# Performance work log

Measured on AMD Instinct MI355X. Metric: run time of the kernel, lower is better.

The kernel has to match this reference:

```python
import jax, jax.numpy as jnp
import numpy as np

N_NODES = 100000
N_EDGES = 3200000
IN_FEATS = 128
H_FEATS = 256
REG_NUM = 1


def _linear_params(key, fan_in, fan_out):
    kw, kb = jax.random.split(key)
    bound = 1.0 / np.sqrt(fan_in)
    W = jax.random.uniform(kw, (fan_out, fan_in), minval=-bound, maxval=bound, dtype=jnp.float32)
    b = jax.random.uniform(kb, (fan_out,), minval=-bound, maxval=bound, dtype=jnp.float32)
    return W, b


def setup_inputs() -> dict:
    key = jax.random.key(0)
    ks = jax.random.split(key, 12)
    node_feat = jax.random.normal(ks[0], (N_NODES, IN_FEATS), dtype=jnp.float32)
    edge_feat = jax.random.normal(ks[1], (N_EDGES, 1), dtype=jnp.float32)
    edge_dst = jax.random.randint(ks[2], (N_EDGES,), 0, N_NODES, dtype=jnp.int64)
    # SAGE layer weights: conv1 maps in_feats+1 -> h_feats; mids map h_feats+1 -> h_feats
    W1, b1 = _linear_params(ks[3], IN_FEATS + 1, H_FEATS)
    Wm1, bm1 = _linear_params(ks[4], H_FEATS + 1, H_FEATS)
    Wm2, bm2 = _linear_params(ks[5], H_FEATS + 1, H_FEATS)
    Wm3, bm3 = _linear_params(ks[6], H_FEATS + 1, H_FEATS)
    Wm4, bm4 = _linear_params(ks[7], H_FEATS + 1, H_FEATS)
    Wr1, br1 = _linear_params(ks[8], H_FEATS + 1, H_FEATS)
    Wr2, br2 = _linear_params(ks[9], H_FEATS, H_FEATS)
    Wr3, br3 = _linear_params(ks[10], H_FEATS, REG_NUM)
    return {
        "node_feat": node_feat, "edge_feat": edge_feat, "edge_dst": edge_dst,
        "W1": W1, "b1": b1,
        "Wm1": Wm1, "bm1": bm1, "Wm2": Wm2, "bm2": bm2,
        "Wm3": Wm3, "bm3": bm3, "Wm4": Wm4, "bm4": bm4,
        "Wr1": Wr1, "br1": br1, "Wr2": Wr2, "br2": br2, "Wr3": Wr3, "br3": br3,
    }


def _sage_layer(hn, he_aggr, W, b):
    # concat [N, d] with [N, 1] then linear
    h_total = jnp.concatenate([hn, he_aggr], axis=1)
    return h_total @ W.T + b


def reference(node_feat, edge_feat, edge_dst,
              W1, b1, Wm1, bm1, Wm2, bm2, Wm3, bm3, Wm4, bm4,
              Wr1, br1, Wr2, br2, Wr3, br3):
    # copy_e + sum: scatter-add edge features onto destination nodes -> [N, 1]
    he_aggr = jax.ops.segment_sum(edge_feat, edge_dst, num_segments=N_NODES)
    h = jax.nn.relu(_sage_layer(node_feat, he_aggr, W1, b1))  # dropout = identity (eval)
    h = jax.nn.relu(_sage_layer(h, he_aggr, Wm1, bm1))
    h = jax.nn.relu(_sage_layer(h, he_aggr, Wm2, bm2))
    h = jax.nn.relu(_sage_layer(h, he_aggr, Wm3, bm3))
    h = jax.nn.relu(_sage_layer(h, he_aggr, Wm4, bm4))
    h = jax.nn.relu(_sage_layer(h, he_aggr, Wr1, br1))
    h = jax.nn.relu(h @ Wr2.T + br2)
    return h @ Wr3.T + br3
```

## Files before the change

kernel.cpp:

```cpp
#include <hip/hip_runtime.h>
#include <hip/hip_bf16.h>

typedef _Float16 half8  __attribute__((ext_vector_type(8)));
typedef _Float16 half4v __attribute__((ext_vector_type(4)));
typedef float    f32x4  __attribute__((ext_vector_type(4)));

#define N_NODES 100000
#define N_EDGES 3200000
#define SH_STRIDE 100096
#define NBUCK 782
#define CAP   5120
#define CHUNK 4096
#define NBIN  782
#define NPK   32

__global__ __launch_bounds__(512) void binpack(
    const float* __restrict__ ef, const int* __restrict__ dst,
    const float* __restrict__ W1,  const float* __restrict__ Wm1,
    const float* __restrict__ Wm2, const float* __restrict__ Wm3,
    const float* __restrict__ Wm4, const float* __restrict__ Wr1,
    const float* __restrict__ Wr2,
    const float* __restrict__ b1,  const float* __restrict__ bm1,
    const float* __restrict__ bm2, const float* __restrict__ bm3,
    const float* __restrict__ bm4, const float* __restrict__ br1,
    const float* __restrict__ br2, const float* __restrict__ wr3,
    const float* __restrict__ br3,
    int* __restrict__ cursor, unsigned* __restrict__ pairs,
    _Float16* __restrict__ Wp, float* __restrict__ park, int do_bin) {

    if (do_bin && blockIdx.x < NBIN) {
        __shared__ int      hist[NBUCK];
        __shared__ int      base[NBUCK];
        __shared__ int      lbase[NBUCK];
        __shared__ int      wsum[8];
        __shared__ unsigned lrec[CHUNK];
        __shared__ int      lslot[CHUNK];
        const int start = blockIdx.x * CHUNK;
        const int tid   = threadIdx.x;
        const int wave  = tid >> 6;
        const int lane  = tid & 63;
        for (int b = tid; b < NBUCK; b += 512) hist[b] = 0;
        __syncthreads();

        int4   dreg[2];
        float4 freg[2];
        int    rnk[2][4];
        #pragma unroll
        for (int it = 0; it < 2; ++it) {
            const int i = start + (it * 512 + tid) * 4;
            if (i < N_EDGES) {
                dreg[it] = *(const int4*)&dst[i];
                freg[it] = *(const float4*)&ef[i];
                rnk[it][0] = atomicAdd(&hist[dreg[it].x >> 7], 1);
                rnk[it][1] = atomicAdd(&hist[dreg[it].y >> 7], 1);
                rnk[it][2] = atomicAdd(&hist[dreg[it].z >> 7], 1);
                rnk[it][3] = atomicAdd(&hist[dreg[it].w >> 7], 1);
            }
        }
        __syncthreads();

        for (int b = tid; b < NBUCK; b += 512) {
            const int c = hist[b];
            base[b] = b * CAP + ((c > 0) ? atomicAdd(&cursor[b], c) : 0);
        }
        const int b0 = 2 * tid, b1 = 2 * tid + 1;
        const int h0 = (b0 < NBUCK) ? hist[b0] : 0;
        const int h1 = (b1 < NBUCK) ? hist[b1] : 0;
        const int psum = h0 + h1;
        int pfx = psum;
        #pragma unroll
        for (int ofs = 1; ofs < 64; ofs <<= 1) {
            const int v = __shfl_up(pfx, ofs);
            if (lane >= ofs) pfx += v;
        }
        if (lane == 63) wsum[wave] = pfx;
        __syncthreads();
        int woff = 0;
        #pragma unroll
        for (int w = 0; w < 8; ++w) woff += (w < wave) ? wsum[w] : 0;
        const int excl = woff + pfx - psum;
        if (b0 < NBUCK) lbase[b0] = excl;
        if (b1 < NBUCK) lbase[b1] = excl + h0;
        __syncthreads();

        #pragma unroll
        for (int it = 0; it < 2; ++it) {
            const int i = start + (it * 512 + tid) * 4;
            if (i < N_EDGES) {
                const int4   d = dreg[it];
                const float4 f = freg[it];
                {   const int bk = d.x >> 7; const int r = rnk[it][0];
                    const int s = lbase[bk] + r; const int g = base[bk] + r;
                    lrec[s]  = (__float_as_uint(f.x) & 0xFFFFFF00u) | (unsigned)(d.x & 127);
                    lslot[s] = (g < (bk + 1) * CAP) ? g : -1; }
                {   const int bk = d.y >> 7; const int r = rnk[it][1];
                    const int s = lbase[bk] + r; const int g = base[bk] + r;
                    lrec[s]  = (__float_as_uint(f.y) & 0xFFFFFF00u) | (unsigned)(d.y & 127);
                    lslot[s] = (g < (bk + 1) * CAP) ? g : -1; }
                {   const int bk = d.z >> 7; const int r = rnk[it][2];
                    const int s = lbase[bk] + r; const int g = base[bk] + r;
                    lrec[s]  = (__float_as_uint(f.z) & 0xFFFFFF00u) | (unsigned)(d.z & 127);
                    lslot[s] = (g < (bk + 1) * CAP) ? g : -1; }
                {   const int bk = d.w >> 7; const int r = rnk[it][3];
                    const int s = lbase[bk] + r; const int g = base[bk] + r;
                    lrec[s]  = (__float_as_uint(f.w) & 0xFFFFFF00u) | (unsigned)(d.w & 127);
                    lslot[s] = (g < (bk + 1) * CAP) ? g : -1; }
            }
        }
        __syncthreads();
        const int total = min(CHUNK, N_EDGES - start);
        for (int s = tid; s < total; s += 512) {
            const int g = lslot[s];
            if (g >= 0) pairs[g] = lrec[s];
        }
    } else {
        const float* srcs[7] = {W1, Wm1, Wm2, Wm3, Wm4, Wr1, Wr2};
        const float* bias[7] = {b1, bm1, bm2, bm3, bm4, br1, br2};
        const int pb  = do_bin ? ((int)blockIdx.x - NBIN) : (int)blockIdx.x;
        const int gid = pb * 512 + threadIdx.x;
        const int gsz = NPK * 512;
        for (int i = gid; i < 425984; i += gsz) {
            int job, w, s, j, lane, e, stride;
            if (i < 32768) {
                job = 0; stride = 129;
                w = i >> 13;
                const int rem = i & 8191;
                s = rem >> 11;
                j = (rem >> 9) & 3;
                lane = (rem >> 3) & 63;
                e = rem & 7;
            } else {
                const int t = i - 32768;
                job = 1 + (t >> 16);
                const int local = t & 65535;
                stride = (job == 6) ? 256 : 257;
                w = local >> 14;
                const int rem = local & 16383;
                s = rem >> 11;
                j = (rem >> 9) & 3;
                lane = (rem >> 3) & 63;
                e = rem & 7;
            }
            const int row = w * 64 + j * 16 + (lane & 15);
            const int col = s * 32 + ((lane >> 4) << 3) + e;
            Wp[i] = (_Float16)srcs[job][row * stride + col];
        }
        for (int i = gid; i < 1536; i += gsz) {
            const int job = i >> 8, row = i & 255;
            const int stride = (job == 0) ? 129 : 257;
            const int kin    = (job == 0) ? 128 : 256;
            park[job * 512 + row] = srcs[job][row * stride + kin];
        }
        for (int i = gid; i < 256; i += gsz) park[6 * 512 + i] = 0.f;
        for (int i = gid; i < 1792; i += gsz)
            park[(i >> 8) * 512 + 256 + (i & 255)] = bias[i >> 8][i & 255];
        for (int i = gid; i < 256; i += gsz) park[3584 + i] = wr3[i];
        if (gid == 0) park[3840] = br3[0];
    }
}

__global__ void scatter4(const float4* __restrict__ ef4,
                         const int4* __restrict__ dst4,
                         float* __restrict__ e) {
    const int n4 = N_EDGES / 4;
    for (int i = blockIdx.x * blockDim.x + threadIdx.x; i < n4;
         i += gridDim.x * blockDim.x) {
        const float4 f = ef4[i];
        const int4   d = dst4[i];
        atomicAdd(&e[d.x], f.x);
        atomicAdd(&e[SH_STRIDE + d.y], f.y);
        atomicAdd(&e[2 * SH_STRIDE + d.z], f.z);
        atomicAdd(&e[3 * SH_STRIDE + d.w], f.w);
    }
}

template<int K>
__device__ __forceinline__ void layer_mm(const _Float16* __restrict__ Wl,
                                         _Float16 (* __restrict__ Hs)[264],
                                         const float* __restrict__ es,
                                         const float* __restrict__ parkl,
                                         int wave, int lane, int m_, int quad) {
    f32x4 acc[4][8];
    #pragma unroll
    for (int jt = 0; jt < 4; ++jt)
        #pragma unroll
        for (int mt = 0; mt < 8; ++mt)
            acc[jt][mt] = (f32x4){0.f, 0.f, 0.f, 0.f};

    const int jb0 = wave * 64 + quad * 4;
    float4 w4[4], bb[4];
    #pragma unroll
    for (int jt = 0; jt < 4; ++jt) {
        w4[jt] = *(const float4*)&parkl[jt * 16 + jb0];
        bb[jt] = *(const float4*)&parkl[256 + jt * 16 + jb0];
    }

    const _Float16* __restrict__ wp = Wl + (size_t)wave * (64 * K) + lane * 8;

    half8 a[4];
    #pragma unroll
    for (int jt = 0; jt < 4; ++jt)
        a[jt] = *(const half8*)(wp + jt * 512);

    half8 b[8];
    #pragma unroll
    for (int mt = 0; mt < 8; ++mt)
        b[mt] = *(const half8*)&Hs[mt * 16 + m_][quad * 8];

    #pragma unroll
    for (int kk = 0; kk < K; kk += 32) {
        const int s = kk >> 5;
        half8 a2[4];
        if (kk + 32 < K) {
            #pragma unroll
            for (int jt = 0; jt < 4; ++jt)
                a2[jt] = *(const half8*)(wp + ((s + 1) * 4 + jt) * 512);
        }
        #pragma unroll
        for (int mt = 0; mt < 8; ++mt) {
            #pragma unroll
            for (int jt = 0; jt < 4; ++jt)
                acc[jt][mt] = __builtin_amdgcn_mfma_f32_16x16x32_f16(
                    a[jt], b[mt], acc[jt][mt], 0, 0, 0);
            if (kk + 32 < K)
                b[mt] = *(const half8*)&Hs[mt * 16 + m_][kk + 32 + quad * 8];
        }
        if (kk + 32 < K) {
            #pragma unroll
            for (int jt = 0; jt < 4; ++jt) a[jt] = a2[jt];
        }
    }
    __syncthreads();

    #pragma unroll
    for (int jt = 0; jt < 4; ++jt) {
        const int jbase = jb0 + jt * 16;
        #pragma unroll
        for (int mt = 0; mt < 8; ++mt) {
            const int node = mt * 16 + m_;
            const float ev = es[node];
            half4v h;
            h[0] = (_Float16)fmaxf(acc[jt][mt][0] + ev * w4[jt].x + bb[jt].x, 0.f);
            h[1] = (_Float16)fmaxf(acc[jt][mt][1] + ev * w4[jt].y + bb[jt].y, 0.f);
            h[2] = (_Float16)fmaxf(acc[jt][mt][2] + ev * w4[jt].z + bb[jt].z, 0.f);
            h[3] = (_Float16)fmaxf(acc[jt][mt][3] + ev * w4[jt].w + bb[jt].w, 0.f);
            *(half4v*)&Hs[node][jbase] = h;
        }
    }
    __syncthreads();
}

__global__ __launch_bounds__(256, 2) void sage_fused(
    const float* __restrict__ node_feat,
    const int* __restrict__ cursor, const unsigned* __restrict__ pairs,
    const float* __restrict__ esh, int nsh,
    const _Float16* __restrict__ Wpack, const float* __restrict__ park,
    float* __restrict__ out) {

    __shared__ _Float16 Hs[128][264];
    __shared__ float esp[528];
    __shared__ float es[128];
    __shared__ float wf[256];
    __shared__ float red[2][128];

    const int tid  = threadIdx.x;
    const int wave = tid >> 6;
    const int lane = tid & 63;
    const int m_   = lane & 15;
    const int quad = lane >> 4;
    const int node0 = blockIdx.x * 128;

    for (int i = tid; i < 528; i += 256) esp[i] = 0.f;

    int cnt = 0;
    if (nsh == 0) cnt = min(cursor[blockIdx.x], CAP);
    __syncthreads();

    for (int idx = tid; idx < 128 * 16; idx += 256) {
        const int row = idx >> 4, g = idx & 15;
        int node = node0 + row; if (node >= N_NODES) node = N_NODES - 1;
        const float4* src = (const float4*)(node_feat + (size_t)node * 128 + g * 8);
        const float4 v0 = src[0], v1 = src[1];
        half8 h;
        h[0] = (_Float16)v0.x; h[1] = (_Float16)v0.y;
        h[2] = (_Float16)v0.z; h[3] = (_Float16)v0.w;
        h[4] = (_Float16)v1.x; h[5] = (_Float16)v1.y;
        h[6] = (_Float16)v1.z; h[7] = (_Float16)v1.w;
        *(half8*)&Hs[row][g * 8] = h;
    }
    if (nsh != 0 && tid < 128) {
        int node = node0 + tid; if (node >= N_NODES) node = N_NODES - 1;
        float s = 0.f;
        for (int sh = 0; sh < nsh; ++sh) s += esh[(size_t)sh * SH_STRIDE + node];
        esp[tid] = s;
    }
    __syncthreads();

    {
        f32x4 acc[4][8];
        #pragma unroll
        for (int jt = 0; jt < 4; ++jt)
            #pragma unroll
            for (int mt = 0; mt < 8; ++mt)
                acc[jt][mt] = (f32x4){0.f, 0.f, 0.f, 0.f};

        const int jb0 = wave * 64 + quad * 4;
        float4 w4[4], bb4[4];
        #pragma unroll
        for (int jt = 0; jt < 4; ++jt) {
            w4[jt]  = *(const float4*)&park[jt * 16 + jb0];
            bb4[jt] = *(const float4*)&park[256 + jt * 16 + jb0];
        }

        const _Float16* __restrict__ wp =
            Wpack + (size_t)wave * (64 * 128) + lane * 8;
        half8 a[4];
        #pragma unroll
        for (int jt = 0; jt < 4; ++jt)
            a[jt] = *(const half8*)(wp + jt * 512);
        half8 b[8];
        #pragma unroll
        for (int mt = 0; mt < 8; ++mt)
            b[mt] = *(const half8*)&Hs[mt * 16 + m_][quad * 8];

        const unsigned* __restrict__ pp = pairs + (size_t)blockIdx.x * CAP;
        const int sh = (tid & 3) * 132;

        #pragma unroll
        for (int kk = 0; kk < 128; kk += 32) {
            const int s = kk >> 5;
            half8 a2[4];
            if (kk + 32 < 128) {
                #pragma unroll
                for (int jt = 0; jt < 4; ++jt)
                    a2[jt] = *(const half8*)(wp + ((s + 1) * 4 + jt) * 512);
            }
            if (nsh == 0) {
                for (int i = tid + (s << 8); i < cnt; i += 1024) {
                    const unsigned p = pp[i];
                    atomicAdd(&esp[sh + (p & 127u)],
                              __uint_as_float(p & 0xFFFFFF00u));
                }
            }
            #pragma unroll
            for (int mt = 0; mt < 8; ++mt) {
                #pragma unroll
                for (int jt = 0; jt < 4; ++jt)
                    acc[jt][mt] = __builtin_amdgcn_mfma_f32_16x16x32_f16(
                        a[jt], b[mt], acc[jt][mt], 0, 0, 0);
                if (kk + 32 < 128)
                    b[mt] = *(const half8*)&Hs[mt * 16 + m_][kk + 32 + quad * 8];
            }
            if (kk + 32 < 128) {
                #pragma unroll
                for (int jt = 0; jt < 4; ++jt) a[jt] = a2[jt];
            }
        }
        __syncthreads();
        if (tid < 128)
            es[tid] = esp[tid] + esp[132 + tid] + esp[264 + tid] + esp[396 + tid];
        __syncthreads();

        #pragma unroll
        for (int jt = 0; jt < 4; ++jt) {
            const int jbase = jb0 + jt * 16;
            #pragma unroll
            for (int mt = 0; mt < 8; ++mt) {
                const int node = mt * 16 + m_;
                const float ev = es[node];
                half4v h;
                h[0] = (_Float16)fmaxf(acc[jt][mt][0] + ev * w4[jt].x + bb4[jt].x, 0.f);
                h[1] = (_Float16)fmaxf(acc[jt][mt][1] + ev * w4[jt].y + bb4[jt].y, 0.f);
                h[2] = (_Float16)fmaxf(acc[jt][mt][2] + ev * w4[jt].z + bb4[jt].z, 0.f);
                h[3] = (_Float16)fmaxf(acc[jt][mt][3] + ev * w4[jt].w + bb4[jt].w, 0.f);
                *(half4v*)&Hs[node][jbase] = h;
            }
        }
        __syncthreads();
    }

    for (int l = 1; l < 7; ++l)
        layer_mm<256>(Wpack + 32768 + (l - 1) * 65536, Hs, es, park + l * 512,
                      wave, lane, m_, quad);

    wf[tid] = park[3584 + tid];
    __syncthreads();
    {
        const int row = tid & 127, seg = tid >> 7;
        const _Float16* hp = &Hs[row][seg * 128];
        const float* wpt = &wf[seg * 128];
        float s = 0.f;
        #pragma unroll
        for (int k = 0; k < 16; ++k) {
            const half8 h = *(const half8*)(hp + k * 8);
            const float* w8 = wpt + k * 8;
            s += (float)h[0] * w8[0] + (float)h[1] * w8[1]
               + (float)h[2] * w8[2] + (float)h[3] * w8[3]
               + (float)h[4] * w8[4] + (float)h[5] * w8[5]
               + (float)h[6] * w8[6] + (float)h[7] * w8[7];
        }
        red[seg][row] = s;
    }
    __syncthreads();
    if (tid < 128) {
        const int node = node0 + tid;
        if (node < N_NODES)
            out[node] = red[0][tid] + red[1][tid] + park[3840];
    }
}

extern "C" void kernel_launch(void* const* d_in, const int* in_sizes, int n_in,
                              void* d_out, int out_size, void* d_ws,
                              size_t ws_size, hipStream_t stream) {
    const float* node_feat = (const float*)d_in[0];
    const float* edge_feat = (const float*)d_in[1];
    const int*   edge_dst  = (const int*)d_in[2];
    const float* W1  = (const float*)d_in[3];  const float* b1  = (const float*)d_in[4];
    const float* Wm1 = (const float*)d_in[5];  const float* bm1 = (const float*)d_in[6];
    const float* Wm2 = (const float*)d_in[7];  const float* bm2 = (const float*)d_in[8];
    const float* Wm3 = (const float*)d_in[9];  const float* bm3 = (const float*)d_in[10];
    const float* Wm4 = (const float*)d_in[11]; const float* bm4 = (const float*)d_in[12];
    const float* Wr1 = (const float*)d_in[13]; const float* br1 = (const float*)d_in[14];
    const float* Wr2 = (const float*)d_in[15]; const float* br2 = (const float*)d_in[16];
    const float* Wr3 = (const float*)d_in[17]; const float* br3 = (const float*)d_in[18];
    float* out = (float*)d_out;

    char* ws = (char*)d_ws;
    int*      cursor = (int*)ws;
    _Float16* Wp     = (_Float16*)(ws + 4096);
    float*    park   = (float*)(ws + 856064);
    unsigned* pairs  = (unsigned*)(ws + 872448);
    float*    esh    = (float*)(ws + 872448);

    const size_t need_bins = 872448 + (size_t)NBUCK * CAP * 4;
    const bool use_bins = (ws_size >= need_bins);

    const int nblk = (N_NODES + 127) / 128;

    if (use_bins) {
        hipMemsetAsync(cursor, 0, NBUCK * sizeof(int), stream);
        binpack<<<NBIN + NPK, 512, 0, stream>>>(
            edge_feat, edge_dst, W1, Wm1, Wm2, Wm3, Wm4, Wr1, Wr2,
            b1, bm1, bm2, bm3, bm4, br1, br2, Wr3, br3,
            cursor, pairs, Wp, park, 1);
        sage_fused<<<nblk, 256, 0, stream>>>(node_feat, cursor, pairs,
                                             nullptr, 0, Wp, park, out);
    } else {
        binpack<<<NPK, 512, 0, stream>>>(
            edge_feat, edge_dst, W1, Wm1, Wm2, Wm3, Wm4, Wr1, Wr2,
            b1, bm1, bm2, bm3, bm4, br1, br2, Wr3, br3,
            cursor, pairs, Wp, park, 0);
        hipMemsetAsync(esh, 0, (size_t)4 * SH_STRIDE * 4, stream);
        scatter4<<<3125, 256, 0, stream>>>((const float4*)edge_feat,
                                           (const int4*)edge_dst, esh);
        sage_fused<<<nblk, 256, 0, stream>>>(node_feat, nullptr, nullptr,
                                             esh, 4, Wp, park, out);
    }
}
```

Baseline: 277.4 us.

## Retile fused SAGE GEMMs as 2x2 wave grid over nodes and output features

Each wave previously computed 64 output features for all 128 nodes, reading the full H tile from LDS. Now the four waves form a 2x2 grid, so each wave handles 64 nodes by 128 features. This halves per-wave LDS reads of the activations and doubles the per-wave weight fragments fetched from global/L2. The weight stream is now prefetched inside the MFMA loop in place of the LDS stream, with bias and edge-weight loads moved into the epilogue loop.

```diff
diff --git a/kernel.cpp b/kernel.cpp
--- a/kernel.cpp
+++ b/kernel.cpp
@@ -180,70 +180,70 @@
                                          const float* __restrict__ es,
                                          const float* __restrict__ parkl,
                                          int wave, int lane, int m_, int quad) {
-    f32x4 acc[4][8];
+    const int wr = wave >> 1, wc = wave & 1;
+    const int row0 = wr * 64;
+
+    f32x4 acc[8][4];
     #pragma unroll
-    for (int jt = 0; jt < 4; ++jt)
-        #pragma unroll
-        for (int mt = 0; mt < 8; ++mt)
+    for (int jt = 0; jt < 8; ++jt)
+        #pragma unroll
+        for (int mt = 0; mt < 4; ++mt)
             acc[jt][mt] = (f32x4){0.f, 0.f, 0.f, 0.f};
 
-    const int jb0 = wave * 64 + quad * 4;
-    float4 w4[4], bb[4];
+    const _Float16* __restrict__ wp = Wl + lane * 8;
+
+    half8 a[8];
     #pragma unroll
-    for (int jt = 0; jt < 4; ++jt) {
-        w4[jt] = *(const float4*)&parkl[jt * 16 + jb0];
-        bb[jt] = *(const float4*)&parkl[256 + jt * 16 + jb0];
-    }
-
-    const _Float16* __restrict__ wp = Wl + (size_t)wave * (64 * K) + lane * 8;
-
-    half8 a[4];
+    for (int jt = 0; jt < 8; ++jt)
+        a[jt] = *(const half8*)(wp + (size_t)(wc * 2 + (jt >> 2)) * (64 * K)
+                                + (jt & 3) * 512);
+
+    half8 b[4];
     #pragma unroll
-    for (int jt = 0; jt < 4; ++jt)
-        a[jt] = *(const half8*)(wp + jt * 512);
-
-    half8 b[8];
-    #pragma unroll
-    for (int mt = 0; mt < 8; ++mt)
-        b[mt] = *(const half8*)&Hs[mt * 16 + m_][quad * 8];
+    for (int mt = 0; mt < 4; ++mt)
+        b[mt] = *(const half8*)&Hs[row0 + mt * 16 + m_][quad * 8];
 
     #pragma unroll
     for (int kk = 0; kk < K; kk += 32) {
         const int s = kk >> 5;
-        half8 a2[4];
+        half8 b2[4];
         if (kk + 32 < K) {
             #pragma unroll
-            for (int jt = 0; jt < 4; ++jt)
-                a2[jt] = *(const half8*)(wp + ((s + 1) * 4 + jt) * 512);
-        }
-        #pragma unroll
-        for (int mt = 0; mt < 8; ++mt) {
-            #pragma unroll
-            for (int jt = 0; jt < 4; ++jt)
+            for (int mt = 0; mt < 4; ++mt)
+                b2[mt] = *(const half8*)&Hs[row0 + mt * 16 + m_][kk + 32 + quad * 8];
+        }
+        #pragma unroll
+        for (int jt = 0; jt < 8; ++jt) {
+            #pragma unroll
+            for (int mt = 0; mt < 4; ++mt)
                 acc[jt][mt] = __builtin_amdgcn_mfma_f32_16x16x32_f16(
                     a[jt], b[mt], acc[jt][mt], 0, 0, 0);
             if (kk + 32 < K)
-                b[mt] = *(const half8*)&Hs[mt * 16 + m_][kk + 32 + quad * 8];
+                a[jt] = *(const half8*)(wp + (size_t)(wc * 2 + (jt >> 2)) * (64 * K)
+                                        + ((s + 1) * 4 + (jt & 3)) * 512);
         }
         if (kk + 32 < K) {
             #pragma unroll
-            for (int jt = 0; jt < 4; ++jt) a[jt] = a2[jt];
-        }
-    }
-    __syncthreads();
-
+            for (int mt = 0; mt < 4; ++mt) b[mt] = b2[mt];
+        }
+    }
+    __syncthreads();
+
+    const int jb0 = wc * 128 + quad * 4;
     #pragma unroll
-    for (int jt = 0; jt < 4; ++jt) {
+    for (int jt = 0; jt < 8; ++jt) {
         const int jbase = jb0 + jt * 16;
-        #pragma unroll
-        for (int mt = 0; mt < 8; ++mt) {
-            const int node = mt * 16 + m_;
+        const float4 w4 = *(const float4*)&parkl[jbase];
+        const float4 bb = *(const float4*)&parkl[256 + jbase];
+        #pragma unroll
+        for (int mt = 0; mt < 4; ++mt) {
+            const int node = row0 + mt * 16 + m_;
             const float ev = es[node];
             half4v h;
-            h[0] = (_Float16)fmaxf(acc[jt][mt][0] + ev * w4[jt].x + bb[jt].x, 0.f);
-            h[1] = (_Float16)fmaxf(acc[jt][mt][1] + ev * w4[jt].y + bb[jt].y, 0.f);
-            h[2] = (_Float16)fmaxf(acc[jt][mt][2] + ev * w4[jt].z + bb[jt].z, 0.f);
-            h[3] = (_Float16)fmaxf(acc[jt][mt][3] + ev * w4[jt].w + bb[jt].w, 0.f);
+            h[0] = (_Float16)fmaxf(acc[jt][mt][0] + ev * w4.x + bb.x, 0.f);
+            h[1] = (_Float16)fmaxf(acc[jt][mt][1] + ev * w4.y + bb.y, 0.f);
+            h[2] = (_Float16)fmaxf(acc[jt][mt][2] + ev * w4.z + bb.z, 0.f);
+            h[3] = (_Float16)fmaxf(acc[jt][mt][3] + ev * w4.w + bb.w, 0.f);
             *(half4v*)&Hs[node][jbase] = h;
         }
     }
@@ -268,6 +268,8 @@
     const int lane = tid & 63;
     const int m_   = lane & 15;
     const int quad = lane >> 4;
+    const int wr   = wave >> 1;
+    const int wc   = wave & 1;
     const int node0 = blockIdx.x * 128;
 
     for (int i = tid; i < 528; i += 256) esp[i] = 0.f;
@@ -297,31 +299,24 @@
     __syncthreads();
 
     {
-        f32x4 acc[4][8];
-        #pragma unroll
-        for (int jt = 0; jt < 4; ++jt)
-            #pragma unroll
-            for (int mt = 0; mt < 8; ++mt)
+        const int row0 = wr * 64;
+        f32x4 acc[8][4];
+        #pragma unroll
+        for (int jt = 0; jt < 8; ++jt)
+            #pragma unroll
+            for (int mt = 0; mt < 4; ++mt)
                 acc[jt][mt] = (f32x4){0.f, 0.f, 0.f, 0.f};
 
-        const int jb0 = wave * 64 + quad * 4;
-        float4 w4[4], bb4[4];
-        #pragma unroll
-        for (int jt = 0; jt < 4; ++jt) {
-            w4[jt]  = *(const float4*)&park[jt * 16 + jb0];
-            bb4[jt] = *(const float4*)&park[256 + jt * 16 + jb0];
-        }
-
-        const _Float16* __restrict__ wp =
-            Wpack + (size_t)wave * (64 * 128) + lane * 8;
-        half8 a[4];
-        #pragma unroll
-        for (int jt = 0; jt < 4; ++jt)
-            a[jt] = *(const half8*)(wp + jt * 512);
-        half8 b[8];
-        #pragma unroll
-        for (int mt = 0; mt < 8; ++mt)
-            b[mt] = *(const half8*)&Hs[mt * 16 + m_][quad * 8];
+        const _Float16* __restrict__ wp = Wpack + lane * 8;
+        half8 a[8];
+        #pragma unroll
+        for (int jt = 0; jt < 8; ++jt)
+            a[jt] = *(const half8*)(wp + (size_t)(wc * 2 + (jt >> 2)) * 8192
+                                    + (jt & 3) * 512);
+        half8 b[4];
+        #pragma unroll
+        for (int mt = 0; mt < 4; ++mt)
+            b[mt] = *(const half8*)&Hs[row0 + mt * 16 + m_][quad * 8];
 
         const unsigned* __restrict__ pp = pairs + (size_t)blockIdx.x * CAP;
         const int sh = (tid & 3) * 132;
@@ -329,11 +324,11 @@
         #pragma unroll
         for (int kk = 0; kk < 128; kk += 32) {
             const int s = kk >> 5;
-            half8 a2[4];
+            half8 b2[4];
             if (kk + 32 < 128) {
                 #pragma unroll
-                for (int jt = 0; jt < 4; ++jt)
-                    a2[jt] = *(const half8*)(wp + ((s + 1) * 4 + jt) * 512);
+                for (int mt = 0; mt < 4; ++mt)
+                    b2[mt] = *(const half8*)&Hs[row0 + mt * 16 + m_][kk + 32 + quad * 8];
             }
             if (nsh == 0) {
                 for (int i = tid + (s << 8); i < cnt; i += 1024) {
@@ -343,17 +338,18 @@
                 }
             }
             #pragma unroll
-            for (int mt = 0; mt < 8; ++mt) {
+            for (int jt = 0; jt < 8; ++jt) {
                 #pragma unroll
-                for (int jt = 0; jt < 4; ++jt)
+                for (int mt = 0; mt < 4; ++mt)
                     acc[jt][mt] = __builtin_amdgcn_mfma_f32_16x16x32_f16(
                         a[jt], b[mt], acc[jt][mt], 0, 0, 0);
                 if (kk + 32 < 128)
-                    b[mt] = *(const half8*)&Hs[mt * 16 + m_][kk + 32 + quad * 8];
+                    a[jt] = *(const half8*)(wp + (size_t)(wc * 2 + (jt >> 2)) * 8192
+                                            + ((s + 1) * 4 + (jt & 3)) * 512);
             }
             if (kk + 32 < 128) {
                 #pragma unroll
-                for (int jt = 0; jt < 4; ++jt) a[jt] = a2[jt];
+                for (int mt = 0; mt < 4; ++mt) b[mt] = b2[mt];
             }
         }
         __syncthreads();
@@ -361,18 +357,21 @@
             es[tid] = esp[tid] + esp[132 + tid] + esp[264 + tid] + esp[396 + tid];
         __syncthreads();
 
-        #pragma unroll
-        for (int jt = 0; jt < 4; ++jt) {
+        const int jb0 = wc * 128 + quad * 4;
+        #pragma unroll
+        for (int jt = 0; jt < 8; ++jt) {
             const int jbase = jb0 + jt * 16;
-            #pragma unroll
-            for (int mt = 0; mt < 8; ++mt) {
-                const int node = mt * 16 + m_;
+            const float4 w4 = *(const float4*)&park[jbase];
+            const float4 bb = *(const float4*)&park[256 + jbase];
+            #pragma unroll
+            for (int mt = 0; mt < 4; ++mt) {
+                const int node = row0 + mt * 16 + m_;
                 const float ev = es[node];
                 half4v h;
-                h[0] = (_Float16)fmaxf(acc[jt][mt][0] + ev * w4[jt].x + bb4[jt].x, 0.f);
-                h[1] = (_Float16)fmaxf(acc[jt][mt][1] + ev * w4[jt].y + bb4[jt].y, 0.f);
-                h[2] = (_Float16)fmaxf(acc[jt][mt][2] + ev * w4[jt].z + bb4[jt].z, 0.f);
-                h[3] = (_Float16)fmaxf(acc[jt][mt][3] + ev * w4[jt].w + bb4[jt].w, 0.f);
+                h[0] = (_Float16)fmaxf(acc[jt][mt][0] + ev * w4.x + bb.x, 0.f);
+                h[1] = (_Float16)fmaxf(acc[jt][mt][1] + ev * w4.y + bb.y, 0.f);
+                h[2] = (_Float16)fmaxf(acc[jt][mt][2] + ev * w4.z + bb.z, 0.f);
+                h[3] = (_Float16)fmaxf(acc[jt][mt][3] + ev * w4.w + bb.w, 0.f);
                 *(half4v*)&Hs[node][jbase] = h;
             }
         }
```

Measured after the change: 301.5 us. +8.7%, slower.
